# Kernel tuning notes

Hardware: AMD Instinct MI355X
Metric: run time of the kernel (lower is better)

## Reference

```python
import jax, jax.numpy as jnp
import numpy as np

N_HOP = 2
KGE_WEIGHT = 0.01
L2_WEIGHT = 1e-7


def setup_inputs() -> dict:
    key = jax.random.key(0)
    ks = jax.random.split(key, 7)
    B, M, NE, NR, D = 16384, 64, 1_000_000, 24, 16
    return {
        "entity_emb": jax.random.normal(ks[0], (NE, D), jnp.float32) * 0.1,
        "relation_emb": jax.random.normal(ks[1], (NR, D * D), jnp.float32) * 0.1,
        "items": jax.random.randint(ks[2], (B,), 0, NE),
        "labels": jax.random.randint(ks[3], (B,), 0, 2),
        "memories_h": jax.random.randint(ks[4], (N_HOP, B, M), 0, NE),
        "memories_r": jax.random.randint(ks[5], (N_HOP, B, M), 0, NR),
        "memories_t": jax.random.randint(ks[6], (N_HOP, B, M), 0, NE),
    }


def reference(entity_emb, relation_emb, items, labels, memories_h, memories_r, memories_t):
    D = entity_emb.shape[-1]
    B, M = memories_h.shape[1], memories_h.shape[2]

    item_emb = entity_emb[items]  # [B, D]
    o_list = []
    kge_acc = jnp.float32(0.0)
    l2_acc = jnp.float32(0.0)

    for hop in range(N_HOP):
        h = entity_emb[memories_h[hop]]                              # [B, M, D]
        r = relation_emb[memories_r[hop]].reshape(B, M, D, D)        # [B, M, D, D]
        t = entity_emb[memories_t[hop]]                              # [B, M, D]

        # key addressing: Rh = r @ h ; probs = <Rh, item>
        Rh = jnp.einsum('bmij,bmj->bmi', r, h)                       # [B, M, D]
        probs = jnp.einsum('bmi,bi->bm', Rh, item_emb)               # [B, M]
        probs = jax.nn.softmax(probs, axis=1)
        o = jnp.einsum('bmd,bm->bd', t, probs)                       # [B, D]
        item_emb = item_emb + o  # 'plus' item update mode
        o_list.append(o)

        # KGE term: sigmoid(h^T R t).mean()
        hRt = jnp.einsum('bmi,bmij,bmj->bm', h, r, t)
        kge_acc = kge_acc + jax.nn.sigmoid(hRt).mean()

        # L2 term
        l2_acc = l2_acc + (h * h).sum() + (t * t).sum() + (r * r).sum()

    # predict (using_all_hops=True)
    y = o_list[-1]
    for i in range(N_HOP - 1):
        y = y + o_list[i]
    logits = (item_emb * y).sum(axis=1)                              # [B]
    scores = jax.nn.sigmoid(logits)

    # stable BCE on sigmoid(logits)
    lab = labels.astype(jnp.float32)
    base_loss = ((1.0 - lab) * logits + jax.nn.softplus(-logits)).mean()
    kge_loss = -KGE_WEIGHT * kge_acc
    l2_loss = L2_WEIGHT * l2_acc
    loss = base_loss + kge_loss + l2_loss
    return scores, loss
```

## Files before the change

kernel.cpp:

```cpp
#include <hip/hip_runtime.h>
#include <math.h>

#define NHOP 2
#define BSZ 16384
#define MSZ 64
#define NREL 24
#define KGE_W 0.01
#define L2_W 1e-7

#define WAVES_PER_BLOCK 4
#define NB_PER_WAVE 2
#define GRID_BLKS (BSZ / (WAVES_PER_BLOCK * NB_PER_WAVE))

typedef float v2f __attribute__((ext_vector_type(2)));

__device__ __forceinline__ float wave_sum(float v) {
#pragma unroll
    for (int off = 32; off > 0; off >>= 1) v += __shfl_xor(v, off, 64);
    return v;
}

__device__ __forceinline__ float wave_max(float v) {
#pragma unroll
    for (int off = 32; off > 0; off >>= 1) v = fmaxf(v, __shfl_xor(v, off, 64));
    return v;
}

__global__ void relsumsq_kernel(const float* __restrict__ rel, float* __restrict__ out) {
    int r = blockIdx.x;
    int lane = threadIdx.x;
    const float4* rp = reinterpret_cast<const float4*>(rel + (size_t)r * 256);
    float4 v = rp[lane];
    float s = v.x * v.x + v.y * v.y + v.z * v.z + v.w * v.w;
    s = wave_sum(s);
    if (lane == 0) out[r] = s;
}

__global__ __launch_bounds__(256) void ripple_kernel(
    const float* __restrict__ ent,
    const float* __restrict__ rel,
    const int* __restrict__ items,
    const int* __restrict__ labels,
    const int* __restrict__ mh,
    const int* __restrict__ mr,
    const int* __restrict__ mt,
    const float* __restrict__ relsq,
    float* __restrict__ scores,
    double* __restrict__ partials)
{
    const int lane = threadIdx.x & 63;
    const int wave = threadIdx.x >> 6;

    float base_loc = 0.f;
    float kge_loc = 0.f;
    float l2_loc = 0.f;

    for (int nb = 0; nb < NB_PER_WAVE; ++nb) {
        const int b = (blockIdx.x * WAVES_PER_BLOCK + wave) * NB_PER_WAVE + nb;

        float item[16], y[16];
        {
            const float4* p4 = reinterpret_cast<const float4*>(ent + (size_t)items[b] * 16);
            float4 a = p4[0], c = p4[1], d4 = p4[2], e = p4[3];
            item[0] = a.x; item[1] = a.y; item[2] = a.z; item[3] = a.w;
            item[4] = c.x; item[5] = c.y; item[6] = c.z; item[7] = c.w;
            item[8] = d4.x; item[9] = d4.y; item[10] = d4.z; item[11] = d4.w;
            item[12] = e.x; item[13] = e.y; item[14] = e.z; item[15] = e.w;
        }
#pragma unroll
        for (int d = 0; d < 16; ++d) y[d] = 0.f;
        const float lab = (float)labels[b];

        for (int hop = 0; hop < NHOP; ++hop) {
            const size_t idx = (size_t)hop * BSZ * MSZ + (size_t)b * MSZ + lane;
            const int ih = mh[idx];
            const int ir = mr[idx];
            const int it = mt[idx];

            v2f ht[16];
            {
                const float4* hp = reinterpret_cast<const float4*>(ent + (size_t)ih * 16);
                const float4* tp = reinterpret_cast<const float4*>(ent + (size_t)it * 16);
#pragma unroll
                for (int q = 0; q < 4; ++q) {
                    float4 hv = hp[q], tv = tp[q];
                    ht[q * 4 + 0] = (v2f){hv.x, tv.x};
                    ht[q * 4 + 1] = (v2f){hv.y, tv.y};
                    ht[q * 4 + 2] = (v2f){hv.z, tv.z};
                    ht[q * 4 + 3] = (v2f){hv.w, tv.w};
                }
            }

            const float4* rp = reinterpret_cast<const float4*>(rel + (size_t)ir * 256);

            v2f sc2 = (v2f){0.f, 0.f};
#pragma unroll
            for (int i = 0; i < 16; ++i) {
                const float4 r0 = rp[4 * i + 0];
                const float4 r1 = rp[4 * i + 1];
                const float4 r2 = rp[4 * i + 2];
                const float4 r3 = rp[4 * i + 3];
                v2f a = (v2f){0.f, 0.f};
                a = __builtin_elementwise_fma((v2f){r0.x, r0.x}, ht[0], a);
                a = __builtin_elementwise_fma((v2f){r0.y, r0.y}, ht[1], a);
                a = __builtin_elementwise_fma((v2f){r0.z, r0.z}, ht[2], a);
                a = __builtin_elementwise_fma((v2f){r0.w, r0.w}, ht[3], a);
                a = __builtin_elementwise_fma((v2f){r1.x, r1.x}, ht[4], a);
                a = __builtin_elementwise_fma((v2f){r1.y, r1.y}, ht[5], a);
                a = __builtin_elementwise_fma((v2f){r1.z, r1.z}, ht[6], a);
                a = __builtin_elementwise_fma((v2f){r1.w, r1.w}, ht[7], a);
                a = __builtin_elementwise_fma((v2f){r2.x, r2.x}, ht[8], a);
                a = __builtin_elementwise_fma((v2f){r2.y, r2.y}, ht[9], a);
                a = __builtin_elementwise_fma((v2f){r2.z, r2.z}, ht[10], a);
                a = __builtin_elementwise_fma((v2f){r2.w, r2.w}, ht[11], a);
                a = __builtin_elementwise_fma((v2f){r3.x, r3.x}, ht[12], a);
                a = __builtin_elementwise_fma((v2f){r3.y, r3.y}, ht[13], a);
                a = __builtin_elementwise_fma((v2f){r3.z, r3.z}, ht[14], a);
                a = __builtin_elementwise_fma((v2f){r3.w, r3.w}, ht[15], a);
                sc2 = __builtin_elementwise_fma(a, (v2f){item[i], ht[i].x}, sc2);
            }

            const float mx = wave_max(sc2.x);
            const float e = __expf(sc2.x - mx);
            const float s = wave_sum(e);
            const float p = e / s;

#pragma unroll
            for (int d = 0; d < 16; ++d) {
                const float od = wave_sum(p * ht[d].y);
                item[d] += od;
                y[d] += od;
            }

            kge_loc += 1.f / (1.f + __expf(-sc2.y));

            v2f l2a = (v2f){0.f, 0.f};
#pragma unroll
            for (int d = 0; d < 16; ++d) l2a = __builtin_elementwise_fma(ht[d], ht[d], l2a);
            l2_loc += relsq[ir] + l2a.x + l2a.y;
        }

        float logit = 0.f;
#pragma unroll
        for (int d = 0; d < 16; ++d) logit = fmaf(item[d], y[d], logit);

        if (lane == 0) {
            scores[b] = 1.f / (1.f + __expf(-logit));
            base_loc += (1.f - lab) * logit + fmaxf(-logit, 0.f) + log1pf(expf(-fabsf(logit)));
        }
    }

    kge_loc = wave_sum(kge_loc);
    l2_loc = wave_sum(l2_loc);

    __shared__ double sred[WAVES_PER_BLOCK][3];
    if (lane == 0) {
        sred[wave][0] = (double)base_loc;
        sred[wave][1] = (double)kge_loc;
        sred[wave][2] = (double)l2_loc;
    }
    __syncthreads();
    if (threadIdx.x < 3) {
        double acc = 0.0;
        for (int w = 0; w < WAVES_PER_BLOCK; ++w) acc += sred[w][threadIdx.x];
        partials[(size_t)blockIdx.x * 3 + threadIdx.x] = acc;
    }
}

__global__ void finalize_kernel(const double* __restrict__ partials, float* __restrict__ out_loss) {
    const int lane = threadIdx.x;
    double b0 = 0.0, b1 = 0.0, b2 = 0.0;
    for (int i = lane; i < GRID_BLKS; i += 64) {
        b0 += partials[(size_t)i * 3 + 0];
        b1 += partials[(size_t)i * 3 + 1];
        b2 += partials[(size_t)i * 3 + 2];
    }
#pragma unroll
    for (int off = 32; off > 0; off >>= 1) {
        b0 += __shfl_xor(b0, off, 64);
        b1 += __shfl_xor(b1, off, 64);
        b2 += __shfl_xor(b2, off, 64);
    }
    if (lane == 0) {
        const double base = b0 / (double)BSZ;
        const double kge = b1 / ((double)BSZ * (double)MSZ);
        const double l2 = b2;
        out_loss[0] = (float)(base - KGE_W * kge + L2_W * l2);
    }
}

extern "C" void kernel_launch(void* const* d_in, const int* in_sizes, int n_in,
                              void* d_out, int out_size, void* d_ws, size_t ws_size,
                              hipStream_t stream) {
    const float* ent    = (const float*)d_in[0];
    const float* rel    = (const float*)d_in[1];
    const int*   items  = (const int*)d_in[2];
    const int*   labels = (const int*)d_in[3];
    const int*   mh     = (const int*)d_in[4];
    const int*   mr     = (const int*)d_in[5];
    const int*   mt     = (const int*)d_in[6];

    float* out = (float*)d_out;
    float* relsq = (float*)d_ws;
    double* partials = (double*)((char*)d_ws + 256);

    relsumsq_kernel<<<NREL, 64, 0, stream>>>(rel, relsq);
    ripple_kernel<<<GRID_BLKS, 256, 0, stream>>>(ent, rel, items, labels, mh, mr, mt,
                                                 relsq, out, partials);
    finalize_kernel<<<1, 64, 0, stream>>>(partials, out + BSZ);
}
```

Before: 462.3 us.

## Process one batch row per wave and issue both hops' gathers upfront

Each wave now handles a single batch element instead of two, which doubles the grid size. All index loads and entity gathers for both hops are issued at the start. The hop-1 relation product R·h is computed before the hop-0 softmax, because it does not depend on the updated item embedding. Only the final dot with the item is deferred. This exposes more memory-level parallelism for the random gathers, at the cost of higher register pressure from holding both hops' h/t data and Rh1 live at once.

New measurement: 398.0 us. -13.9%, faster.

```diff
diff --git a/kernel.cpp b/kernel.cpp
--- a/kernel.cpp
+++ b/kernel.cpp
@@ -9,8 +9,7 @@
 #define L2_W 1e-7
 
 #define WAVES_PER_BLOCK 4
-#define NB_PER_WAVE 2
-#define GRID_BLKS (BSZ / (WAVES_PER_BLOCK * NB_PER_WAVE))
+#define GRID_BLKS (BSZ / WAVES_PER_BLOCK)
 
 typedef float v2f __attribute__((ext_vector_type(2)));
 
@@ -50,104 +49,157 @@
 {
     const int lane = threadIdx.x & 63;
     const int wave = threadIdx.x >> 6;
+    const int b = blockIdx.x * WAVES_PER_BLOCK + wave;
+
+    const size_t i0 = (size_t)b * MSZ + lane;
+    const size_t i1 = (size_t)BSZ * MSZ + i0;
+    const int ih0 = mh[i0], ir0 = mr[i0], it0 = mt[i0];
+    const int ih1 = mh[i1], ir1 = mr[i1], it1 = mt[i1];
+
+    const float4* h0p = reinterpret_cast<const float4*>(ent + (size_t)ih0 * 16);
+    const float4* t0p = reinterpret_cast<const float4*>(ent + (size_t)it0 * 16);
+    const float4* h1p = reinterpret_cast<const float4*>(ent + (size_t)ih1 * 16);
+    const float4* t1p = reinterpret_cast<const float4*>(ent + (size_t)it1 * 16);
+    const float4* ip  = reinterpret_cast<const float4*>(ent + (size_t)items[b] * 16);
+
+    float4 h0q[4], t0q[4], h1q[4], t1q[4], iq[4];
+#pragma unroll
+    for (int q = 0; q < 4; ++q) h0q[q] = h0p[q];
+#pragma unroll
+    for (int q = 0; q < 4; ++q) t0q[q] = t0p[q];
+#pragma unroll
+    for (int q = 0; q < 4; ++q) h1q[q] = h1p[q];
+#pragma unroll
+    for (int q = 0; q < 4; ++q) t1q[q] = t1p[q];
+#pragma unroll
+    for (int q = 0; q < 4; ++q) iq[q] = ip[q];
+
+    v2f ht0[16], ht1[16];
+#pragma unroll
+    for (int q = 0; q < 4; ++q) {
+        ht0[q * 4 + 0] = (v2f){h0q[q].x, t0q[q].x};
+        ht0[q * 4 + 1] = (v2f){h0q[q].y, t0q[q].y};
+        ht0[q * 4 + 2] = (v2f){h0q[q].z, t0q[q].z};
+        ht0[q * 4 + 3] = (v2f){h0q[q].w, t0q[q].w};
+        ht1[q * 4 + 0] = (v2f){h1q[q].x, t1q[q].x};
+        ht1[q * 4 + 1] = (v2f){h1q[q].y, t1q[q].y};
+        ht1[q * 4 + 2] = (v2f){h1q[q].z, t1q[q].z};
+        ht1[q * 4 + 3] = (v2f){h1q[q].w, t1q[q].w};
+    }
+    float item[16], y[16];
+#pragma unroll
+    for (int q = 0; q < 4; ++q) {
+        item[q * 4 + 0] = iq[q].x; item[q * 4 + 1] = iq[q].y;
+        item[q * 4 + 2] = iq[q].z; item[q * 4 + 3] = iq[q].w;
+    }
+#pragma unroll
+    for (int d = 0; d < 16; ++d) y[d] = 0.f;
+
+    const float4* r0p = reinterpret_cast<const float4*>(rel + (size_t)ir0 * 256);
+    v2f sc0 = (v2f){0.f, 0.f};
+#pragma unroll
+    for (int i = 0; i < 16; ++i) {
+        const float4 r0 = r0p[4 * i + 0];
+        const float4 r1 = r0p[4 * i + 1];
+        const float4 r2 = r0p[4 * i + 2];
+        const float4 r3 = r0p[4 * i + 3];
+        v2f a = (v2f){0.f, 0.f};
+        a = __builtin_elementwise_fma((v2f){r0.x, r0.x}, ht0[0], a);
+        a = __builtin_elementwise_fma((v2f){r0.y, r0.y}, ht0[1], a);
+        a = __builtin_elementwise_fma((v2f){r0.z, r0.z}, ht0[2], a);
+        a = __builtin_elementwise_fma((v2f){r0.w, r0.w}, ht0[3], a);
+        a = __builtin_elementwise_fma((v2f){r1.x, r1.x}, ht0[4], a);
+        a = __builtin_elementwise_fma((v2f){r1.y, r1.y}, ht0[5], a);
+        a = __builtin_elementwise_fma((v2f){r1.z, r1.z}, ht0[6], a);
+        a = __builtin_elementwise_fma((v2f){r1.w, r1.w}, ht0[7], a);
+        a = __builtin_elementwise_fma((v2f){r2.x, r2.x}, ht0[8], a);
+        a = __builtin_elementwise_fma((v2f){r2.y, r2.y}, ht0[9], a);
+        a = __builtin_elementwise_fma((v2f){r2.z, r2.z}, ht0[10], a);
+        a = __builtin_elementwise_fma((v2f){r2.w, r2.w}, ht0[11], a);
+        a = __builtin_elementwise_fma((v2f){r3.x, r3.x}, ht0[12], a);
+        a = __builtin_elementwise_fma((v2f){r3.y, r3.y}, ht0[13], a);
+        a = __builtin_elementwise_fma((v2f){r3.z, r3.z}, ht0[14], a);
+        a = __builtin_elementwise_fma((v2f){r3.w, r3.w}, ht0[15], a);
+        sc0 = __builtin_elementwise_fma(a, (v2f){item[i], ht0[i].x}, sc0);
+    }
+
+    const float4* r1p = reinterpret_cast<const float4*>(rel + (size_t)ir1 * 256);
+    float Rh1[16];
+    float hRt1 = 0.f;
+#pragma unroll
+    for (int i = 0; i < 16; ++i) {
+        const float4 r0 = r1p[4 * i + 0];
+        const float4 r1 = r1p[4 * i + 1];
+        const float4 r2 = r1p[4 * i + 2];
+        const float4 r3 = r1p[4 * i + 3];
+        v2f a = (v2f){0.f, 0.f};
+        a = __builtin_elementwise_fma((v2f){r0.x, r0.x}, ht1[0], a);
+        a = __builtin_elementwise_fma((v2f){r0.y, r0.y}, ht1[1], a);
+        a = __builtin_elementwise_fma((v2f){r0.z, r0.z}, ht1[2], a);
+        a = __builtin_elementwise_fma((v2f){r0.w, r0.w}, ht1[3], a);
+        a = __builtin_elementwise_fma((v2f){r1.x, r1.x}, ht1[4], a);
+        a = __builtin_elementwise_fma((v2f){r1.y, r1.y}, ht1[5], a);
+        a = __builtin_elementwise_fma((v2f){r1.z, r1.z}, ht1[6], a);
+        a = __builtin_elementwise_fma((v2f){r1.w, r1.w}, ht1[7], a);
+        a = __builtin_elementwise_fma((v2f){r2.x, r2.x}, ht1[8], a);
+        a = __builtin_elementwise_fma((v2f){r2.y, r2.y}, ht1[9], a);
+        a = __builtin_elementwise_fma((v2f){r2.z, r2.z}, ht1[10], a);
+        a = __builtin_elementwise_fma((v2f){r2.w, r2.w}, ht1[11], a);
+        a = __builtin_elementwise_fma((v2f){r3.x, r3.x}, ht1[12], a);
+        a = __builtin_elementwise_fma((v2f){r3.y, r3.y}, ht1[13], a);
+        a = __builtin_elementwise_fma((v2f){r3.z, r3.z}, ht1[14], a);
+        a = __builtin_elementwise_fma((v2f){r3.w, r3.w}, ht1[15], a);
+        Rh1[i] = a.x;
+        hRt1 = fmaf(ht1[i].x, a.y, hRt1);
+    }
+
+    {
+        const float mx = wave_max(sc0.x);
+        const float e = __expf(sc0.x - mx);
+        const float s = wave_sum(e);
+        const float p = e / s;
+#pragma unroll
+        for (int d = 0; d < 16; ++d) {
+            const float od = wave_sum(p * ht0[d].y);
+            item[d] += od;
+            y[d] += od;
+        }
+    }
+
+    {
+        float score = 0.f;
+#pragma unroll
+        for (int i = 0; i < 16; ++i) score = fmaf(item[i], Rh1[i], score);
+        const float mx = wave_max(score);
+        const float e = __expf(score - mx);
+        const float s = wave_sum(e);
+        const float p = e / s;
+#pragma unroll
+        for (int d = 0; d < 16; ++d) {
+            const float od = wave_sum(p * ht1[d].y);
+            item[d] += od;
+            y[d] += od;
+        }
+    }
+
+    float kge_loc = 1.f / (1.f + __expf(-sc0.y)) + 1.f / (1.f + __expf(-hRt1));
+    v2f l2a = (v2f){0.f, 0.f};
+#pragma unroll
+    for (int d = 0; d < 16; ++d) {
+        l2a = __builtin_elementwise_fma(ht0[d], ht0[d], l2a);
+        l2a = __builtin_elementwise_fma(ht1[d], ht1[d], l2a);
+    }
+    float l2_loc = relsq[ir0] + relsq[ir1] + l2a.x + l2a.y;
+
+    float logit = 0.f;
+#pragma unroll
+    for (int d = 0; d < 16; ++d) logit = fmaf(item[d], y[d], logit);
 
     float base_loc = 0.f;
-    float kge_loc = 0.f;
-    float l2_loc = 0.f;
-
-    for (int nb = 0; nb < NB_PER_WAVE; ++nb) {
-        const int b = (blockIdx.x * WAVES_PER_BLOCK + wave) * NB_PER_WAVE + nb;
-
-        float item[16], y[16];
-        {
-            const float4* p4 = reinterpret_cast<const float4*>(ent + (size_t)items[b] * 16);
-            float4 a = p4[0], c = p4[1], d4 = p4[2], e = p4[3];
-            item[0] = a.x; item[1] = a.y; item[2] = a.z; item[3] = a.w;
-            item[4] = c.x; item[5] = c.y; item[6] = c.z; item[7] = c.w;
-            item[8] = d4.x; item[9] = d4.y; item[10] = d4.z; item[11] = d4.w;
-            item[12] = e.x; item[13] = e.y; item[14] = e.z; item[15] = e.w;
-        }
-#pragma unroll
-        for (int d = 0; d < 16; ++d) y[d] = 0.f;
+    if (lane == 0) {
+        scores[b] = 1.f / (1.f + __expf(-logit));
         const float lab = (float)labels[b];
-
-        for (int hop = 0; hop < NHOP; ++hop) {
-            const size_t idx = (size_t)hop * BSZ * MSZ + (size_t)b * MSZ + lane;
-            const int ih = mh[idx];
-            const int ir = mr[idx];
-            const int it = mt[idx];
-
-            v2f ht[16];
-            {
-                const float4* hp = reinterpret_cast<const float4*>(ent + (size_t)ih * 16);
-                const float4* tp = reinterpret_cast<const float4*>(ent + (size_t)it * 16);
-#pragma unroll
-                for (int q = 0; q < 4; ++q) {
-                    float4 hv = hp[q], tv = tp[q];
-                    ht[q * 4 + 0] = (v2f){hv.x, tv.x};
-                    ht[q * 4 + 1] = (v2f){hv.y, tv.y};
-                    ht[q * 4 + 2] = (v2f){hv.z, tv.z};
-                    ht[q * 4 + 3] = (v2f){hv.w, tv.w};
-                }
-            }
-
-            const float4* rp = reinterpret_cast<const float4*>(rel + (size_t)ir * 256);
-
-            v2f sc2 = (v2f){0.f, 0.f};
-#pragma unroll
-            for (int i = 0; i < 16; ++i) {
-                const float4 r0 = rp[4 * i + 0];
-                const float4 r1 = rp[4 * i + 1];
-                const float4 r2 = rp[4 * i + 2];
-                const float4 r3 = rp[4 * i + 3];
-                v2f a = (v2f){0.f, 0.f};
-                a = __builtin_elementwise_fma((v2f){r0.x, r0.x}, ht[0], a);
-                a = __builtin_elementwise_fma((v2f){r0.y, r0.y}, ht[1], a);
-                a = __builtin_elementwise_fma((v2f){r0.z, r0.z}, ht[2], a);
-                a = __builtin_elementwise_fma((v2f){r0.w, r0.w}, ht[3], a);
-                a = __builtin_elementwise_fma((v2f){r1.x, r1.x}, ht[4], a);
-                a = __builtin_elementwise_fma((v2f){r1.y, r1.y}, ht[5], a);
-                a = __builtin_elementwise_fma((v2f){r1.z, r1.z}, ht[6], a);
-                a = __builtin_elementwise_fma((v2f){r1.w, r1.w}, ht[7], a);
-                a = __builtin_elementwise_fma((v2f){r2.x, r2.x}, ht[8], a);
-                a = __builtin_elementwise_fma((v2f){r2.y, r2.y}, ht[9], a);
-                a = __builtin_elementwise_fma((v2f){r2.z, r2.z}, ht[10], a);
-                a = __builtin_elementwise_fma((v2f){r2.w, r2.w}, ht[11], a);
-                a = __builtin_elementwise_fma((v2f){r3.x, r3.x}, ht[12], a);
-                a = __builtin_elementwise_fma((v2f){r3.y, r3.y}, ht[13], a);
-                a = __builtin_elementwise_fma((v2f){r3.z, r3.z}, ht[14], a);
-                a = __builtin_elementwise_fma((v2f){r3.w, r3.w}, ht[15], a);
-                sc2 = __builtin_elementwise_fma(a, (v2f){item[i], ht[i].x}, sc2);
-            }
-
-            const float mx = wave_max(sc2.x);
-            const float e = __expf(sc2.x - mx);
-            const float s = wave_sum(e);
-            const float p = e / s;
-
-#pragma unroll
-            for (int d = 0; d < 16; ++d) {
-                const float od = wave_sum(p * ht[d].y);
-                item[d] += od;
-                y[d] += od;
-            }
-
-            kge_loc += 1.f / (1.f + __expf(-sc2.y));
-
-            v2f l2a = (v2f){0.f, 0.f};
-#pragma unroll
-            for (int d = 0; d < 16; ++d) l2a = __builtin_elementwise_fma(ht[d], ht[d], l2a);
-            l2_loc += relsq[ir] + l2a.x + l2a.y;
-        }
-
-        float logit = 0.f;
-#pragma unroll
-        for (int d = 0; d < 16; ++d) logit = fmaf(item[d], y[d], logit);
-
-        if (lane == 0) {
-            scores[b] = 1.f / (1.f + __expf(-logit));
-            base_loc += (1.f - lab) * logit + fmaxf(-logit, 0.f) + log1pf(expf(-fabsf(logit)));
-        }
+        base_loc = (1.f - lab) * logit + fmaxf(-logit, 0.f) + log1pf(expf(-fabsf(logit)));
     }
 
     kge_loc = wave_sum(kge_loc);
```
